# Performance work log

Measured on AMD Instinct MI355X. Metric: run time of the kernel, lower is better.

Reference implementation:

```python
import jax, jax.numpy as jnp
import numpy as np

VOCAB, EMB, HID, TEMP = 10000, 256, 512, 0.5
EPS = 1e-20


def _lstm(x_seq, h0, c0, Wih, Whh, b):
    # x_seq: [T, B, E]; PyTorch gate order i, f, g, o
    def step(carry, x):
        h, c = carry
        gates = x @ Wih + h @ Whh + b
        i, f, g, o = jnp.split(gates, 4, axis=-1)
        c = jax.nn.sigmoid(f) * c + jax.nn.sigmoid(i) * jnp.tanh(g)
        h = jax.nn.sigmoid(o) * jnp.tanh(c)
        return (h, c), h
    (hT, cT), hs = jax.lax.scan(step, (h0, c0), x_seq)
    return hs, hT, cT


def setup_inputs() -> dict:
    key = jax.random.key(0)
    ks = jax.random.split(key, 16)
    B, T = 32, 128
    s = 0.02
    input_ids = jax.random.randint(ks[0], (B, T), 0, VOCAB, dtype=jnp.int32)
    mask = jax.random.randint(ks[1], (B, T), 0, 2, dtype=jnp.int32)
    U = jax.random.uniform(ks[2], (T, B, VOCAB), dtype=jnp.float32)
    gumbel_noise = -jnp.log(-jnp.log(U + EPS) + EPS)
    return {
        'input_ids': input_ids,
        'my_attention_mask': mask,
        'enc_embed': s * jax.random.normal(ks[3], (VOCAB, EMB), jnp.float32),
        'enc_Wih': s * jax.random.normal(ks[4], (EMB, 4 * HID), jnp.float32),
        'enc_Whh': s * jax.random.normal(ks[5], (HID, 4 * HID), jnp.float32),
        'enc_b': jnp.zeros((4 * HID,), jnp.float32),
        'dec_embed': s * jax.random.normal(ks[6], (VOCAB, EMB), jnp.float32),
        'dec_Wih': s * jax.random.normal(ks[7], (EMB, 4 * HID), jnp.float32),
        'dec_Whh': s * jax.random.normal(ks[8], (HID, 4 * HID), jnp.float32),
        'dec_b': jnp.zeros((4 * HID,), jnp.float32),
        'fc_W': s * jax.random.normal(ks[9], (HID, VOCAB), jnp.float32),
        'fc_b': jnp.zeros((VOCAB,), jnp.float32),
        'rand_init': jax.random.uniform(ks[10], (T, B, VOCAB), dtype=jnp.float32),
        'gumbel_noise': gumbel_noise,
    }


def reference(input_ids, my_attention_mask, enc_embed, enc_Wih, enc_Whh, enc_b,
              dec_embed, dec_Wih, dec_Whh, dec_b, fc_W, fc_b,
              rand_init, gumbel_noise):
    B, T = input_ids.shape
    mask = my_attention_mask                      # [B, T]
    tokens = input_ids.T                          # [T, B] (torch.t of view)

    h0 = jnp.zeros((B, HID), jnp.float32)
    # Encoder over full sequence
    _, hT, cT = _lstm(enc_embed[tokens], h0, h0, enc_Wih, enc_Whh, enc_b)
    # Decoder: teacher-forced on tokens[0:T-1] -> outputs for steps t=1..T-1
    hs, _, _ = _lstm(dec_embed[tokens[:-1]], hT, cT, dec_Wih, dec_Whh, dec_b)
    logits = hs @ fc_W + fc_b                     # [T-1, B, V]

    # Mask-driven compaction: outputs[sum(mask[j,:t]), j] = logits[t-1, j] where mask[j,t]==1
    excl = jnp.cumsum(mask, axis=1) - mask        # exclusive prefix sum [B, T]
    pos = excl[:, 1:]                             # [B, T-1]
    valid = mask[:, 1:] > 0
    pos_use = jnp.where(valid, pos, T)            # out-of-range -> dropped
    jj = jnp.broadcast_to(jnp.arange(B)[:, None], pos_use.shape)
    outputs = rand_init.at[pos_use, jj].set(jnp.swapaxes(logits, 0, 1), mode='drop')  # [T, B, V]

    # Hard gumbel-softmax with straight-through
    y = jax.nn.softmax((outputs + gumbel_noise) / TEMP, axis=-1)
    y_hard = jax.nn.one_hot(jnp.argmax(y, axis=-1), VOCAB, dtype=y.dtype)
    gs = jax.lax.stop_gradient(y_hard - y) + y    # [T, B, V]

    # Re-expand: masked positions take compacted gumbel rows, unmasked take token one-hots
    gathered = gs[excl, jnp.arange(B)[:, None]]   # [B, T, V]
    tok_oh = jax.nn.one_hot(input_ids, VOCAB, dtype=jnp.float32)
    onehots = jnp.where((mask > 0)[..., None], gathered, tok_oh)  # [B, T, V]
    return onehots.reshape(-1, VOCAB)             # dense form of the sparse inputs_embeds
```

## Files before the change

kernel.cpp:

```cpp
#include <hip/hip_runtime.h>
#include <hip/hip_bf16.h>
#include <math.h>

#define BB 32
#define TT 128
#define TD 127
#define EMB 256
#define HID 512
#define G4 2048
#define NV 10000
#define NB 64
#define UPB 8

typedef __attribute__((ext_vector_type(8))) short short8v;
typedef __attribute__((ext_vector_type(4))) float f32x4;

__device__ __forceinline__ unsigned short bf16_rne(float x){
    unsigned int u = __float_as_uint(x);
    u += 0x7fffu + ((u >> 16) & 1u);
    return (unsigned short)(u >> 16);
}
__device__ __forceinline__ float bf16f(unsigned short h){
    return __uint_as_float(((unsigned int)h) << 16);
}

__global__ __launch_bounds__(256) void gemm_x(const int* __restrict__ ids,
        const float* __restrict__ embed, const float* __restrict__ W,
        const float* __restrict__ bias, float* __restrict__ X, int M)
{
    __shared__ float As[16][128];
    __shared__ float Bs[16][128];
    __shared__ int toks[128];
    const int tid = threadIdx.x;
    const int m0 = blockIdx.y * 128, n0 = blockIdx.x * 128;
    if (tid < 128) {
        int mr = m0 + tid, tk = 0;
        if (mr < M) { int t = mr >> 5, b = mr & 31; tk = ids[b*TT + t]; }
        toks[tid] = tk;
    }
    __syncthreads();
    float acc[8][8] = {};
    const int ty = tid >> 4, tx = tid & 15;
    for (int kt = 0; kt < EMB; kt += 16) {
        #pragma unroll
        for (int i = 0; i < 2; i++) {
            int idx = tid*2 + i;
            int row = idx >> 2, k4 = (idx & 3)*4;
            float4 a = *(const float4*)&embed[(size_t)toks[row]*EMB + kt + k4];
            As[k4+0][row] = a.x; As[k4+1][row] = a.y; As[k4+2][row] = a.z; As[k4+3][row] = a.w;
        }
        #pragma unroll
        for (int i = 0; i < 2; i++) {
            int idx = tid*2 + i;
            int kr = idx >> 5, c4 = (idx & 31)*4;
            *(float4*)&Bs[kr][c4] = *(const float4*)&W[(size_t)(kt+kr)*G4 + n0 + c4];
        }
        __syncthreads();
        #pragma unroll
        for (int k = 0; k < 16; k++) {
            float a8[8], b8[8];
            #pragma unroll
            for (int i = 0; i < 8; i++) a8[i] = As[k][ty*8+i];
            #pragma unroll
            for (int j = 0; j < 8; j++) b8[j] = Bs[k][tx*8+j];
            #pragma unroll
            for (int i = 0; i < 8; i++) {
                #pragma unroll
                for (int j = 0; j < 8; j++)
                    acc[i][j] = fmaf(a8[i], b8[j], acc[i][j]);
            }
        }
        __syncthreads();
    }
    #pragma unroll
    for (int i = 0; i < 8; i++) {
        int mr = m0 + ty*8 + i;
        if (mr < M) {
            int tt = mr >> 5, bb2 = mr & 31;
            #pragma unroll
            for (int j = 0; j < 8; j++) {
                int nc = n0 + tx*8 + j;
                X[((size_t)tt*G4 + nc)*BB + bb2] = acc[i][j] + bias[nc];
            }
        }
    }
}

__global__ __launch_bounds__(512) void lstm_persist(
        const float* __restrict__ Xenc, const float* __restrict__ Xdec,
        const float* __restrict__ Whh_e, const float* __restrict__ Whh_d,
        unsigned int* __restrict__ h_pk,
        float* __restrict__ hs,
        int* __restrict__ flags)
{
    __shared__ float smem[10272];
    float* partials = smem;
    float* xbuf     = smem + 9216;

    const int tid = threadIdx.x;
    const int bid = blockIdx.x;
    const int u0  = bid*UPB;
    const int w   = tid >> 6;
    const int l   = tid & 63;
    const int rl  = l & 15;
    const int kg  = (l >> 4) * 8;
    const int r4  = (l >> 4) * 4;

    short8v wH_n0k0, wH_n0k1, wH_n1k0, wH_n1k1;
    short8v wL_n0k0, wL_n0k1, wL_n1k0, wL_n1k1;

    #define BW(WH, WL, KB, CO) do { _Pragma("unroll") \
        for (int j = 0; j < 8; ++j) { \
            float wv = partials[((KB)+j)*32 + (CO) + rl]; \
            unsigned short h2 = bf16_rne(wv); \
            WH[j] = (short)h2; \
            WL[j] = (short)bf16_rne(wv - bf16f(h2)); \
        } } while(0)

    #define STAGE_BUILD(SRC) do { \
        for (int c = 0; c < 4; ++c) { \
            int k0 = c*128; \
            __syncthreads(); \
            for (int i = tid; i < 4096; i += 512) { \
                int kl = i >> 5, n = i & 31; \
                partials[kl*32 + n] = SRC[(size_t)(k0+kl)*G4 + (size_t)((n>>3)*512 + u0 + (n&7))]; \
            } \
            __syncthreads(); \
            if ((w >> 1) == c) { \
                int kb0 = w*64 - k0 + kg; \
                BW(wH_n0k0, wL_n0k0, kb0,      0); \
                BW(wH_n0k1, wL_n0k1, kb0 + 32, 0); \
                BW(wH_n1k0, wL_n1k0, kb0,     16); \
                BW(wH_n1k1, wL_n1k1, kb0 + 32,16); \
            } \
        } \
        __syncthreads(); } while(0)

    STAGE_BUILD(Whh_e);

    {
        for (int i = tid; i < 1024; i += 512) {
            int row = i & 31, n = i >> 5;
            xbuf[row*33 + n] = Xenc[(size_t)((n>>3)*512 + u0 + (n&7))*32 + row];
        }
        __syncthreads();
    }

    float c_reg = 0.f;
    const int gb = tid >> 3, gul = tid & 7;

    for (int gstep = 0; gstep < TT + TD; ++gstep) {
        const bool enc = gstep < TT;
        const int t = enc ? gstep : gstep - TT;

        f32x4 acc00 = {0,0,0,0}, acc01 = {0,0,0,0}, acc10 = {0,0,0,0}, acc11 = {0,0,0,0};
        if (gstep > 0) {
            const unsigned int* hp = h_pk + (size_t)(gstep & 1)*16384;
            short8v aH_m0k0, aH_m0k1, aH_m1k0, aH_m1k1;
            short8v aL_m0k0, aL_m0k1, aL_m1k0, aL_m1k1;
            #define LOAD_A(AH, AL, MT, KS) do { \
                unsigned int pv[8]; \
                int kbase = w*64 + (KS)*32 + kg; \
                int brow = (MT)*16 + rl; \
                _Pragma("unroll") \
                for (int j = 0; j < 8; ++j) \
                    pv[j] = __hip_atomic_load(&hp[(kbase+j)*32 + brow], \
                                __ATOMIC_RELAXED, __HIP_MEMORY_SCOPE_AGENT); \
                _Pragma("unroll") \
                for (int j = 0; j < 8; ++j) { \
                    AH[j] = (short)(pv[j] & 0xffffu); \
                    AL[j] = (short)(pv[j] >> 16); \
                } } while(0)
            LOAD_A(aH_m0k0, aL_m0k0, 0, 0); LOAD_A(aH_m0k1, aL_m0k1, 0, 1);
            LOAD_A(aH_m1k0, aL_m1k0, 1, 0); LOAD_A(aH_m1k1, aL_m1k1, 1, 1);
            #define MM6(ACC, AH0, AH1, AL0, AL1, WH0, WH1, WL0, WL1) do { \
                ACC = __builtin_amdgcn_mfma_f32_16x16x32_bf16(AH0, WH0, ACC, 0,0,0); \
                ACC = __builtin_amdgcn_mfma_f32_16x16x32_bf16(AH1, WH1, ACC, 0,0,0); \
                ACC = __builtin_amdgcn_mfma_f32_16x16x32_bf16(AL0, WH0, ACC, 0,0,0); \
                ACC = __builtin_amdgcn_mfma_f32_16x16x32_bf16(AL1, WH1, ACC, 0,0,0); \
                ACC = __builtin_amdgcn_mfma_f32_16x16x32_bf16(AH0, WL0, ACC, 0,0,0); \
                ACC = __builtin_amdgcn_mfma_f32_16x16x32_bf16(AH1, WL1, ACC, 0,0,0); \
            } while(0)
            MM6(acc00, aH_m0k0, aH_m0k1, aL_m0k0, aL_m0k1, wH_n0k0, wH_n0k1, wL_n0k0, wL_n0k1);
            MM6(acc01, aH_m0k0, aH_m0k1, aL_m0k0, aL_m0k1, wH_n1k0, wH_n1k1, wL_n1k0, wL_n1k1);
            MM6(acc10, aH_m1k0, aH_m1k1, aL_m1k0, aL_m1k1, wH_n0k0, wH_n0k1, wL_n0k0, wL_n0k1);
            MM6(acc11, aH_m1k0, aH_m1k1, aL_m1k0, aL_m1k1, wH_n1k0, wH_n1k1, wL_n1k0, wL_n1k1);
        }
        #pragma unroll
        for (int j = 0; j < 4; ++j) {
            partials[(w*32 +      r4 + j)*36 +      rl] = acc00[j];
            partials[(w*32 +      r4 + j)*36 + 16 + rl] = acc01[j];
            partials[(w*32 + 16 + r4 + j)*36 +      rl] = acc10[j];
            partials[(w*32 + 16 + r4 + j)*36 + 16 + rl] = acc11[j];
        }
        __syncthreads();

        float hv = 0.f;
        if (tid < 256) {
            float pre[4];
            #pragma unroll
            for (int g = 0; g < 4; ++g) {
                float s = xbuf[gb*33 + g*8 + gul];
                #pragma unroll
                for (int ww = 0; ww < 8; ++ww)
                    s += partials[(ww*32 + gb)*36 + g*8 + gul];
                pre[g] = s;
            }
            float iv = 1.f/(1.f + expf(-pre[0]));
            float fv = 1.f/(1.f + expf(-pre[1]));
            float gv = tanhf(pre[2]);
            float ov = 1.f/(1.f + expf(-pre[3]));
            c_reg = fmaf(fv, c_reg, iv*gv);
            hv = ov * tanhf(c_reg);
            unsigned short hh = bf16_rne(hv);
            unsigned short hl = bf16_rne(hv - bf16f(hh));
            unsigned int pk = (unsigned int)hh | ((unsigned int)hl << 16);
            __hip_atomic_store(&h_pk[(size_t)((gstep+1) & 1)*16384 + (u0+gul)*32 + gb],
                               pk, __ATOMIC_RELAXED, __HIP_MEMORY_SCOPE_AGENT);
        }
        __syncthreads();
        if (gstep < TT + TD - 1 && tid == 0)
            __hip_atomic_store(&flags[bid], gstep + 1,
                               __ATOMIC_RELAXED, __HIP_MEMORY_SCOPE_AGENT);
        if (!enc && tid < 256)
            hs[((size_t)t*BB + gb)*HID + u0 + gul] = hv;
        if (gstep == TT + TD - 1) break;

        if (gstep == TT - 1) STAGE_BUILD(Whh_d);

        {
            int tn = gstep + 1 < TT ? gstep + 1 : gstep + 1 - TT;
            const float* Xt = (gstep + 1 < TT ? Xenc : Xdec) + (size_t)tn*G4*BB;
            for (int i = tid; i < 1024; i += 512) {
                int row = i & 31, n = i >> 5;
                xbuf[row*33 + n] = Xt[(size_t)((n>>3)*512 + u0 + (n&7))*32 + row];
            }
        }
        if (tid < NB) {
            while (__hip_atomic_load(&flags[tid], __ATOMIC_RELAXED,
                                     __HIP_MEMORY_SCOPE_AGENT) <= gstep) {}
        }
        __syncthreads();
        asm volatile("" ::: "memory");
    }
}

__global__ void transpose_fc(const float* __restrict__ W, float* __restrict__ Wt)
{
    __shared__ float tile[32][33];
    int v0 = blockIdx.x*32, k0 = blockIdx.y*32;
    int tx = threadIdx.x, ty = threadIdx.y;
    #pragma unroll
    for (int r = 0; r < 32; r += 8) {
        int k = k0 + ty + r, v = v0 + tx;
        tile[ty+r][tx] = (v < NV) ? W[(size_t)k*NV + v] : 0.f;
    }
    __syncthreads();
    #pragma unroll
    for (int r = 0; r < 32; r += 8) {
        int v = v0 + ty + r, k = k0 + tx;
        if (v < NV) Wt[(size_t)v*HID + k] = tile[tx][ty+r];
    }
}

__global__ void wnorm(const float* __restrict__ W, const float* __restrict__ bvec,
                      unsigned int* __restrict__ scal)
{
    int v = blockIdx.x*256 + threadIdx.x;
    if (v < NV) {
        float s = 0.f;
        for (int k = 0; k < HID; k++) { float w = W[(size_t)k*NV + v]; s = fmaf(w, w, s); }
        atomicMax(&scal[0], __float_as_uint(s));
        atomicMax(&scal[1], __float_as_uint(fabsf(bvec[v])));
    }
}

__global__ void hnorm(const float* __restrict__ hs, unsigned int* __restrict__ scal)
{
    int r = blockIdx.x, lane = threadIdx.x;
    float s = 0.f;
    for (int k = lane; k < HID; k += 64) { float x = hs[(size_t)r*HID + k]; s = fmaf(x, x, s); }
    for (int o = 32; o; o >>= 1) s += __shfl_down(s, o);
    if (lane == 0) atomicMax(&scal[2], __float_as_uint(s));
}

__global__ void routing(const int* __restrict__ ids, const int* __restrict__ mask,
                        int* __restrict__ exclk, int* __restrict__ winner)
{
    int b = blockIdx.x;
    __shared__ int pre[TT];
    int t = threadIdx.x;
    if (t == 0) { int s = 0; for (int i = 0; i < TT; i++) { pre[i] = s; s += mask[b*TT+i]; } }
    __syncthreads();
    exclk[b*TT + t] = pre[t];
    if (mask[b*TT + t] == 0) winner[b*TT + t] = ids[b*TT + t];
}

__global__ __launch_bounds__(256) void rowmax(const int* __restrict__ mask,
        const int* __restrict__ exclk, const float* __restrict__ gum, float* __restrict__ Mr)
{
    int row = blockIdx.x, b = row >> 7, t = row & 127;
    if (t == 0 || mask[row] == 0) return;
    int k = exclk[row];
    const float* g = gum + ((size_t)k*BB + b)*NV;
    float m = -1e30f;
    for (int v = threadIdx.x; v < NV; v += 256) m = fmaxf(m, g[v]);
    __shared__ float red[256];
    red[threadIdx.x] = m; __syncthreads();
    for (int s = 128; s; s >>= 1) {
        if (threadIdx.x < s) red[threadIdx.x] = fmaxf(red[threadIdx.x], red[threadIdx.x+s]);
        __syncthreads();
    }
    if (threadIdx.x == 0) Mr[row] = red[0];
}

__global__ __launch_bounds__(256) void cand_argmax(const int* __restrict__ mask,
        const int* __restrict__ exclk, const float* __restrict__ gum,
        const float* __restrict__ rinit, const float* __restrict__ hs,
        const float* __restrict__ Wt, const float* __restrict__ fcb,
        const float* __restrict__ Mr, const unsigned int* __restrict__ scal,
        int* __restrict__ winner)
{
    int row = blockIdx.x, b = row >> 7, t = row & 127;
    if (mask[row] == 0) return;
    int tid = threadIdx.x;
    __shared__ float red[256];
    __shared__ int idxr[256];
    __shared__ int list[256];
    __shared__ int wcnt[4];

    if (t == 0) {
        const float* g  = gum   + (size_t)b*NV;
        const float* r0 = rinit + (size_t)b*NV;
        float bs = -1e30f; int bv = 0x7fffffff;
        for (int v = tid; v < NV; v += 256) {
            float sc = r0[v] + g[v];
            if (sc > bs) { bs = sc; bv = v; }
        }
        red[tid] = bs; idxr[tid] = bv; __syncthreads();
        for (int s = 128; s; s >>= 1) {
            if (tid < s) {
                if (red[tid+s] > red[tid] || (red[tid+s] == red[tid] && idxr[tid+s] < idxr[tid])) {
                    red[tid] = red[tid+s]; idxr[tid] = idxr[tid+s];
                }
            }
            __syncthreads();
        }
        if (tid == 0) winner[row] = idxr[0];
        return;
    }

    int k = exclk[row];
    const float* g    = gum + ((size_t)k*BB + b)*NV;
    const float* hrow = hs + ((size_t)(t-1)*BB + b)*HID;
    float bound = sqrtf(__uint_as_float(scal[0])) * sqrtf(__uint_as_float(scal[2]))
                + __uint_as_float(scal[1]);
    float thr = Mr[row] - 2.0f*bound*1.05f - 1e-6f;

    float curS = -1e30f; int curV = 0x7fffffff;
    int wv = tid >> 6, lane = tid & 63;
    for (int v0 = 0; v0 < NV; v0 += 256) {
        int v = v0 + tid;
        bool ok = (v < NV) && (g[v] >= thr);
        unsigned long long mb = __ballot(ok);
        if (lane == 0) wcnt[wv] = __popcll(mb);
        __syncthreads();
        int off = 0;
        #pragma unroll
        for (int w = 0; w < 4; w++) if (w < wv) off += wcnt[w];
        int tot = wcnt[0] + wcnt[1] + wcnt[2] + wcnt[3];
        if (ok) {
            int pos = off + __popcll(mb & ((1ull << lane) - 1ull));
            list[pos] = v;
        }
        __syncthreads();
        for (int ci = 0; ci < tot; ci++) {
            int vc = list[ci];
            float p = 0.f;
            for (int k2 = tid; k2 < HID; k2 += 256)
                p = fmaf(hrow[k2], Wt[(size_t)vc*HID + k2], p);
            red[tid] = p; __syncthreads();
            for (int s = 128; s; s >>= 1) {
                if (tid < s) red[tid] += red[tid+s];
                __syncthreads();
            }
            if (tid == 0) {
                float sc = (red[0] + fcb[vc]) + g[vc];
                if (sc > curS || (sc == curS && vc < curV)) { curS = sc; curV = vc; }
            }
            __syncthreads();
        }
    }
    if (tid == 0) winner[row] = curV;
}

__global__ __launch_bounds__(256) void write_out(const int* __restrict__ winner,
                                                 float* __restrict__ out)
{
    int row = blockIdx.x;
    int win = winner[row];
    float4* o = (float4*)(out + (size_t)row*NV);
    int tid = threadIdx.x;
    #pragma unroll
    for (int i = 0; i < 10; i++) {
        int idx = tid + i*256;
        if (idx < 2500) {
            int vb = idx*4;
            float4 val = {0.f, 0.f, 0.f, 0.f};
            if (win >= vb && win < vb+4) ((float*)&val)[win - vb] = 1.0f;
            o[idx] = val;
        }
    }
}

extern "C" void kernel_launch(void* const* d_in, const int* in_sizes, int n_in,
                              void* d_out, int out_size, void* d_ws, size_t ws_size,
                              hipStream_t stream)
{
    const int*   ids   = (const int*)d_in[0];
    const int*   mask  = (const int*)d_in[1];
    const float* eEmb  = (const float*)d_in[2];
    const float* eWih  = (const float*)d_in[3];
    const float* eWhh  = (const float*)d_in[4];
    const float* eB    = (const float*)d_in[5];
    const float* dEmb  = (const float*)d_in[6];
    const float* dWih  = (const float*)d_in[7];
    const float* dWhh  = (const float*)d_in[8];
    const float* dB    = (const float*)d_in[9];
    const float* fcW   = (const float*)d_in[10];
    const float* fcb   = (const float*)d_in[11];
    const float* rinit = (const float*)d_in[12];
    const float* gum   = (const float*)d_in[13];
    float* out = (float*)d_out;

    float* wsf = (float*)d_ws;
    size_t off = 0;
    float* Xenc = wsf + off; off += (size_t)TT*BB*G4;
    float* Xdec = wsf + off; off += (size_t)TD*BB*G4;
    unsigned int* h_pk = (unsigned int*)(wsf + off); off += 2*(size_t)BB*HID;
    float* hs   = wsf + off; off += (size_t)TD*BB*HID;
    float* fcWt = wsf + off; off += (size_t)NV*HID;
    float* Mr   = wsf + off; off += 4096;
    unsigned int* scal = (unsigned int*)(wsf + off); off += 8;
    int* flags  = (int*)(wsf + off); off += NB;
    int* exclk  = (int*)(wsf + off); off += 4096;
    int* winner = (int*)(wsf + off); off += 4096;

    hipMemsetAsync(scal,  0, 8*sizeof(int), stream);
    hipMemsetAsync(flags, 0, NB*sizeof(int), stream);

    dim3 gblk(16, 32);
    gemm_x<<<gblk, 256, 0, stream>>>(ids, eEmb, eWih, eB, Xenc, TT*BB);
    gemm_x<<<gblk, 256, 0, stream>>>(ids, dEmb, dWih, dB, Xdec, TD*BB);
    transpose_fc<<<dim3(313,16), dim3(32,8), 0, stream>>>(fcW, fcWt);
    wnorm<<<40, 256, 0, stream>>>(fcW, fcb, scal);
    routing<<<32, 128, 0, stream>>>(ids, mask, exclk, winner);

    lstm_persist<<<NB, 512, 0, stream>>>(Xenc, Xdec, eWhh, dWhh, h_pk, hs, flags);

    hnorm<<<TD*BB, 64, 0, stream>>>(hs, scal);
    rowmax<<<4096, 256, 0, stream>>>(mask, exclk, gum, Mr);
    cand_argmax<<<4096, 256, 0, stream>>>(mask, exclk, gum, rinit, hs, fcWt, fcb, Mr, scal, winner);
    write_out<<<4096, 256, 0, stream>>>(winner, out);
}
```

Before: 1.152 ms.

## Overlap independent precompute with persistent LSTM via worker blocks in same launch

Adds 192 worker blocks to the persistent LSTM grid. While the recurrent blocks run the encoder, the workers do the decoder input GEMM, the fc weight transpose, the weight norm and the gumbel row maxima. The LSTM blocks wait on a completion counter before they read decoder inputs, and the x-buffer is now double-buffered. Routing, hnorm, candidate argmax and output write are merged into one kernel that computes a per-row h norm bound. This removes several launches and their serial tails, at the risk that the workers contend with the latency-sensitive recurrent blocks or that the grid does not fit co-resident.

New measurement: 1.004 ms. -12.8%, faster.

```diff
diff --git a/kernel.cpp b/kernel.cpp
--- a/kernel.cpp
+++ b/kernel.cpp
@@ -10,7 +10,16 @@
 #define G4 2048
 #define NV 10000
 #define NB 64
+#define NWK 192
+#define GRID_UBER (NB + NWK)
 #define UPB 8
+#define NT_STEPS (TT + TD)
+
+#define NJOB_DEC 512
+#define NJOB_TR  313
+#define NJOB_WN  20
+#define NJOB_RM  4096
+#define NJOBS (NJOB_DEC + NJOB_TR + NJOB_WN + NJOB_RM)
 
 typedef __attribute__((ext_vector_type(8))) short short8v;
 typedef __attribute__((ext_vector_type(4))) float f32x4;
@@ -87,34 +96,162 @@
 }
 
 __global__ __launch_bounds__(512) void lstm_persist(
-        const float* __restrict__ Xenc, const float* __restrict__ Xdec,
+        const float* __restrict__ Xenc, float* __restrict__ Xdec,
         const float* __restrict__ Whh_e, const float* __restrict__ Whh_d,
         unsigned int* __restrict__ h_pk,
         float* __restrict__ hs,
-        int* __restrict__ flags)
+        int* __restrict__ flags,
+        int* __restrict__ decdone,
+        const int* __restrict__ ids, const float* __restrict__ dEmb,
+        const float* __restrict__ dWih, const float* __restrict__ dB,
+        const float* __restrict__ fcW, float* __restrict__ fcWt,
+        const float* __restrict__ fcb, const int* __restrict__ mask,
+        const float* __restrict__ gum, float* __restrict__ Mr,
+        unsigned int* __restrict__ scal)
 {
-    __shared__ float smem[10272];
+    __shared__ float smem[11392];
+    const int tid = threadIdx.x;
+    const int bid = blockIdx.x;
+
+    if (bid >= NB) {
+        const int wid = bid - NB;
+        for (int job = wid; job < NJOBS; job += NWK) {
+            if (job < NJOB_DEC) {
+                const int my = job >> 4, nx = job & 15;
+                const int m0 = my*128, n0 = nx*128;
+                const int M = TD*BB;
+                float* As = smem;
+                float* Bs = smem + 2048;
+                int* toks = (int*)(smem + 4096);
+                if (tid < 128) {
+                    int mr = m0 + tid, tk = 0;
+                    if (mr < M) { int t = mr >> 5, b2 = mr & 31; tk = ids[b2*TT + t]; }
+                    toks[tid] = tk;
+                }
+                __syncthreads();
+                float acc[4][8] = {};
+                const int ty = tid >> 4, tx = tid & 15;
+                for (int kt = 0; kt < EMB; kt += 16) {
+                    {
+                        int row = tid >> 2, k4 = (tid & 3)*4;
+                        float4 a = *(const float4*)&dEmb[(size_t)toks[row]*EMB + kt + k4];
+                        As[(k4+0)*128+row] = a.x; As[(k4+1)*128+row] = a.y;
+                        As[(k4+2)*128+row] = a.z; As[(k4+3)*128+row] = a.w;
+                    }
+                    {
+                        int kr = tid >> 5, c4 = (tid & 31)*4;
+                        *(float4*)&Bs[kr*128 + c4] =
+                            *(const float4*)&dWih[(size_t)(kt+kr)*G4 + n0 + c4];
+                    }
+                    __syncthreads();
+                    #pragma unroll
+                    for (int k = 0; k < 16; k++) {
+                        float a4[4], b8[8];
+                        #pragma unroll
+                        for (int i = 0; i < 4; i++) a4[i] = As[k*128 + ty*4+i];
+                        #pragma unroll
+                        for (int j = 0; j < 8; j++) b8[j] = Bs[k*128 + tx*8+j];
+                        #pragma unroll
+                        for (int i = 0; i < 4; i++) {
+                            #pragma unroll
+                            for (int j = 0; j < 8; j++)
+                                acc[i][j] = fmaf(a4[i], b8[j], acc[i][j]);
+                        }
+                    }
+                    __syncthreads();
+                }
+                #pragma unroll
+                for (int i = 0; i < 4; i++) {
+                    int mr = m0 + ty*4 + i;
+                    if (mr < M) {
+                        int t = mr >> 5, b2 = mr & 31;
+                        #pragma unroll
+                        for (int j = 0; j < 8; j++) {
+                            int nc = n0 + tx*8 + j;
+                            Xdec[((size_t)t*G4 + nc)*BB + b2] = acc[i][j] + dB[nc];
+                        }
+                    }
+                }
+                __syncthreads();
+                if (tid == 0)
+                    __hip_atomic_fetch_add(decdone, 1,
+                        __ATOMIC_RELEASE, __HIP_MEMORY_SCOPE_AGENT);
+            } else if (job < NJOB_DEC + NJOB_TR) {
+                const int v0 = (job - NJOB_DEC)*32;
+                float* tile = smem;
+                for (int k0 = 0; k0 < HID; k0 += 16) {
+                    {
+                        int kk = tid >> 5, vv = tid & 31;
+                        int v = v0 + vv;
+                        tile[kk*33 + vv] = (v < NV) ? fcW[(size_t)(k0+kk)*NV + v] : 0.f;
+                    }
+                    __syncthreads();
+                    {
+                        int vy = tid >> 4, kx = tid & 15;
+                        int v = v0 + vy;
+                        if (v < NV) fcWt[(size_t)v*HID + k0 + kx] = tile[kx*33 + vy];
+                    }
+                    __syncthreads();
+                }
+            } else if (job < NJOB_DEC + NJOB_TR + NJOB_WN) {
+                int v = (job - NJOB_DEC - NJOB_TR)*512 + tid;
+                if (v < NV) {
+                    float s = 0.f;
+                    for (int k = 0; k < HID; k++) {
+                        float x = fcW[(size_t)k*NV + v]; s = fmaf(x, x, s);
+                    }
+                    atomicMax(&scal[0], __float_as_uint(s));
+                    atomicMax(&scal[1], __float_as_uint(fabsf(fcb[v])));
+                }
+            } else {
+                const int row = job - NJOB_DEC - NJOB_TR - NJOB_WN;
+                const int b = row >> 7, t = row & 127;
+                const int mrow = mask[row];
+                if (t != 0 && mrow != 0) {
+                    int* wk = (int*)&smem[520];
+                    int mi = (tid < TT) ? mask[b*TT + tid] : 0;
+                    unsigned long long bal = __ballot(tid < t && mi != 0);
+                    if ((tid & 63) == 0) wk[tid >> 6] = __popcll(bal);
+                    __syncthreads();
+                    int k = wk[0] + wk[1];
+                    __syncthreads();
+                    const float* g = gum + ((size_t)k*BB + b)*NV;
+                    float m = -1e30f;
+                    for (int v = tid; v < NV; v += 512) m = fmaxf(m, g[v]);
+                    float* red = smem;
+                    red[tid] = m; __syncthreads();
+                    for (int s = 256; s; s >>= 1) {
+                        if (tid < s) red[tid] = fmaxf(red[tid], red[tid+s]);
+                        __syncthreads();
+                    }
+                    if (tid == 0) Mr[row] = red[0];
+                    __syncthreads();
+                }
+            }
+        }
+        return;
+    }
+
     float* partials = smem;
     float* xbuf     = smem + 9216;
 
-    const int tid = threadIdx.x;
-    const int bid = blockIdx.x;
     const int u0  = bid*UPB;
     const int w   = tid >> 6;
     const int l   = tid & 63;
     const int rl  = l & 15;
     const int kg  = (l >> 4) * 8;
     const int r4  = (l >> 4) * 4;
+    const int gb  = tid >> 3, gul = tid & 7;
 
     short8v wH_n0k0, wH_n0k1, wH_n1k0, wH_n1k1;
     short8v wL_n0k0, wL_n0k1, wL_n1k0, wL_n1k1;
 
     #define BW(WH, WL, KB, CO) do { _Pragma("unroll") \
         for (int j = 0; j < 8; ++j) { \
-            float wv = partials[((KB)+j)*32 + (CO) + rl]; \
-            unsigned short h2 = bf16_rne(wv); \
-            WH[j] = (short)h2; \
-            WL[j] = (short)bf16_rne(wv - bf16f(h2)); \
+            float wv2 = partials[((KB)+j)*32 + (CO) + rl]; \
+            unsigned short htop = bf16_rne(wv2); \
+            WH[j] = (short)htop; \
+            WL[j] = (short)bf16_rne(wv2 - bf16f(htop)); \
         } } while(0)
 
     #define STAGE_BUILD(SRC) do { \
@@ -140,16 +277,24 @@
 
     {
         for (int i = tid; i < 1024; i += 512) {
-            int row = i & 31, n = i >> 5;
-            xbuf[row*33 + n] = Xenc[(size_t)((n>>3)*512 + u0 + (n&7))*32 + row];
+            int row2 = i & 31, n = i >> 5;
+            xbuf[row2*33 + n] = Xenc[(size_t)((n>>3)*512 + u0 + (n&7))*32 + row2];
         }
         __syncthreads();
     }
 
     float c_reg = 0.f;
-    const int gb = tid >> 3, gul = tid & 7;
-
-    for (int gstep = 0; gstep < TT + TD; ++gstep) {
+
+    #define MM6(ACC, AH0, AH1, AL0, AL1, WH0, WH1, WL0, WL1) do { \
+        ACC = __builtin_amdgcn_mfma_f32_16x16x32_bf16(AH0, WH0, ACC, 0,0,0); \
+        ACC = __builtin_amdgcn_mfma_f32_16x16x32_bf16(AH1, WH1, ACC, 0,0,0); \
+        ACC = __builtin_amdgcn_mfma_f32_16x16x32_bf16(AL0, WH0, ACC, 0,0,0); \
+        ACC = __builtin_amdgcn_mfma_f32_16x16x32_bf16(AL1, WH1, ACC, 0,0,0); \
+        ACC = __builtin_amdgcn_mfma_f32_16x16x32_bf16(AH0, WL0, ACC, 0,0,0); \
+        ACC = __builtin_amdgcn_mfma_f32_16x16x32_bf16(AH1, WL1, ACC, 0,0,0); \
+    } while(0)
+
+    for (int gstep = 0; gstep < NT_STEPS; ++gstep) {
         const bool enc = gstep < TT;
         const int t = enc ? gstep : gstep - TT;
 
@@ -173,14 +318,6 @@
                 } } while(0)
             LOAD_A(aH_m0k0, aL_m0k0, 0, 0); LOAD_A(aH_m0k1, aL_m0k1, 0, 1);
             LOAD_A(aH_m1k0, aL_m1k0, 1, 0); LOAD_A(aH_m1k1, aL_m1k1, 1, 1);
-            #define MM6(ACC, AH0, AH1, AL0, AL1, WH0, WH1, WL0, WL1) do { \
-                ACC = __builtin_amdgcn_mfma_f32_16x16x32_bf16(AH0, WH0, ACC, 0,0,0); \
-                ACC = __builtin_amdgcn_mfma_f32_16x16x32_bf16(AH1, WH1, ACC, 0,0,0); \
-                ACC = __builtin_amdgcn_mfma_f32_16x16x32_bf16(AL0, WH0, ACC, 0,0,0); \
-                ACC = __builtin_amdgcn_mfma_f32_16x16x32_bf16(AL1, WH1, ACC, 0,0,0); \
-                ACC = __builtin_amdgcn_mfma_f32_16x16x32_bf16(AH0, WL0, ACC, 0,0,0); \
-                ACC = __builtin_amdgcn_mfma_f32_16x16x32_bf16(AH1, WL1, ACC, 0,0,0); \
-            } while(0)
             MM6(acc00, aH_m0k0, aH_m0k1, aL_m0k0, aL_m0k1, wH_n0k0, wH_n0k1, wL_n0k0, wL_n0k1);
             MM6(acc01, aH_m0k0, aH_m0k1, aL_m0k0, aL_m0k1, wH_n1k0, wH_n1k1, wL_n1k0, wL_n1k1);
             MM6(acc10, aH_m1k0, aH_m1k1, aL_m1k0, aL_m1k1, wH_n0k0, wH_n0k1, wL_n0k0, wL_n0k1);
@@ -199,12 +336,12 @@
         if (tid < 256) {
             float pre[4];
             #pragma unroll
-            for (int g = 0; g < 4; ++g) {
-                float s = xbuf[gb*33 + g*8 + gul];
+            for (int gg = 0; gg < 4; ++gg) {
+                float s = xbuf[(gstep & 1)*1056 + gb*33 + gg*8 + gul];
                 #pragma unroll
                 for (int ww = 0; ww < 8; ++ww)
-                    s += partials[(ww*32 + gb)*36 + g*8 + gul];
-                pre[g] = s;
+                    s += partials[(ww*32 + gb)*36 + gg*8 + gul];
+                pre[gg] = s;
             }
             float iv = 1.f/(1.f + expf(-pre[0]));
             float fv = 1.f/(1.f + expf(-pre[1]));
@@ -219,21 +356,31 @@
                                pk, __ATOMIC_RELAXED, __HIP_MEMORY_SCOPE_AGENT);
         }
         __syncthreads();
-        if (gstep < TT + TD - 1 && tid == 0)
+        if (gstep < NT_STEPS - 1 && tid == 0)
             __hip_atomic_store(&flags[bid], gstep + 1,
                                __ATOMIC_RELAXED, __HIP_MEMORY_SCOPE_AGENT);
         if (!enc && tid < 256)
             hs[((size_t)t*BB + gb)*HID + u0 + gul] = hv;
-        if (gstep == TT + TD - 1) break;
+        if (gstep == NT_STEPS - 1) break;
 
         if (gstep == TT - 1) STAGE_BUILD(Whh_d);
 
         {
+            if (gstep + 1 == TT) {
+                if (tid == 0) {
+                    while (__hip_atomic_load(decdone, __ATOMIC_RELAXED,
+                                             __HIP_MEMORY_SCOPE_AGENT) < NJOB_DEC)
+                        __builtin_amdgcn_s_sleep(8);
+                }
+                __syncthreads();
+                __builtin_amdgcn_fence(__ATOMIC_ACQUIRE, "agent");
+            }
             int tn = gstep + 1 < TT ? gstep + 1 : gstep + 1 - TT;
-            const float* Xt = (gstep + 1 < TT ? Xenc : Xdec) + (size_t)tn*G4*BB;
+            const float* Xt = (gstep + 1 < TT ? Xenc : (const float*)Xdec) + (size_t)tn*G4*BB;
             for (int i = tid; i < 1024; i += 512) {
-                int row = i & 31, n = i >> 5;
-                xbuf[row*33 + n] = Xt[(size_t)((n>>3)*512 + u0 + (n&7))*32 + row];
+                int row2 = i & 31, n = i >> 5;
+                xbuf[((gstep+1) & 1)*1056 + row2*33 + n] =
+                    Xt[(size_t)((n>>3)*512 + u0 + (n&7))*32 + row2];
             }
         }
         if (tid < NB) {
@@ -245,91 +392,25 @@
     }
 }
 
-__global__ void transpose_fc(const float* __restrict__ W, float* __restrict__ Wt)
+__global__ __launch_bounds__(256) void cand_write(
+        const int* __restrict__ ids, const int* __restrict__ mask,
+        const float* __restrict__ gum, const float* __restrict__ rinit,
+        const float* __restrict__ hs, const float* __restrict__ Wt,
+        const float* __restrict__ fcb, const float* __restrict__ Mr,
+        const unsigned int* __restrict__ scal, float* __restrict__ out)
 {
-    __shared__ float tile[32][33];
-    int v0 = blockIdx.x*32, k0 = blockIdx.y*32;
-    int tx = threadIdx.x, ty = threadIdx.y;
-    #pragma unroll
-    for (int r = 0; r < 32; r += 8) {
-        int k = k0 + ty + r, v = v0 + tx;
-        tile[ty+r][tx] = (v < NV) ? W[(size_t)k*NV + v] : 0.f;
-    }
-    __syncthreads();
-    #pragma unroll
-    for (int r = 0; r < 32; r += 8) {
-        int v = v0 + ty + r, k = k0 + tx;
-        if (v < NV) Wt[(size_t)v*HID + k] = tile[tx][ty+r];
-    }
-}
-
-__global__ void wnorm(const float* __restrict__ W, const float* __restrict__ bvec,
-                      unsigned int* __restrict__ scal)
-{
-    int v = blockIdx.x*256 + threadIdx.x;
-    if (v < NV) {
-        float s = 0.f;
-        for (int k = 0; k < HID; k++) { float w = W[(size_t)k*NV + v]; s = fmaf(w, w, s); }
-        atomicMax(&scal[0], __float_as_uint(s));
-        atomicMax(&scal[1], __float_as_uint(fabsf(bvec[v])));
-    }
-}
-
-__global__ void hnorm(const float* __restrict__ hs, unsigned int* __restrict__ scal)
-{
-    int r = blockIdx.x, lane = threadIdx.x;
-    float s = 0.f;
-    for (int k = lane; k < HID; k += 64) { float x = hs[(size_t)r*HID + k]; s = fmaf(x, x, s); }
-    for (int o = 32; o; o >>= 1) s += __shfl_down(s, o);
-    if (lane == 0) atomicMax(&scal[2], __float_as_uint(s));
-}
-
-__global__ void routing(const int* __restrict__ ids, const int* __restrict__ mask,
-                        int* __restrict__ exclk, int* __restrict__ winner)
-{
-    int b = blockIdx.x;
-    __shared__ int pre[TT];
-    int t = threadIdx.x;
-    if (t == 0) { int s = 0; for (int i = 0; i < TT; i++) { pre[i] = s; s += mask[b*TT+i]; } }
-    __syncthreads();
-    exclk[b*TT + t] = pre[t];
-    if (mask[b*TT + t] == 0) winner[b*TT + t] = ids[b*TT + t];
-}
-
-__global__ __launch_bounds__(256) void rowmax(const int* __restrict__ mask,
-        const int* __restrict__ exclk, const float* __restrict__ gum, float* __restrict__ Mr)
-{
-    int row = blockIdx.x, b = row >> 7, t = row & 127;
-    if (t == 0 || mask[row] == 0) return;
-    int k = exclk[row];
-    const float* g = gum + ((size_t)k*BB + b)*NV;
-    float m = -1e30f;
-    for (int v = threadIdx.x; v < NV; v += 256) m = fmaxf(m, g[v]);
-    __shared__ float red[256];
-    red[threadIdx.x] = m; __syncthreads();
-    for (int s = 128; s; s >>= 1) {
-        if (threadIdx.x < s) red[threadIdx.x] = fmaxf(red[threadIdx.x], red[threadIdx.x+s]);
-        __syncthreads();
-    }
-    if (threadIdx.x == 0) Mr[row] = red[0];
-}
-
-__global__ __launch_bounds__(256) void cand_argmax(const int* __restrict__ mask,
-        const int* __restrict__ exclk, const float* __restrict__ gum,
-        const float* __restrict__ rinit, const float* __restrict__ hs,
-        const float* __restrict__ Wt, const float* __restrict__ fcb,
-        const float* __restrict__ Mr, const unsigned int* __restrict__ scal,
-        int* __restrict__ winner)
-{
-    int row = blockIdx.x, b = row >> 7, t = row & 127;
-    if (mask[row] == 0) return;
-    int tid = threadIdx.x;
+    const int row = blockIdx.x, b = row >> 7, t = row & 127;
+    const int tid = threadIdx.x;
     __shared__ float red[256];
     __shared__ int idxr[256];
     __shared__ int list[256];
     __shared__ int wcnt[4];
-
-    if (t == 0) {
+    __shared__ int winsh;
+
+    int win;
+    if (mask[row] == 0) {
+        win = ids[b*TT + t];
+    } else if (t == 0) {
         const float* g  = gum   + (size_t)b*NV;
         const float* r0 = rinit + (size_t)b*NV;
         float bs = -1e30f; int bv = 0x7fffffff;
@@ -346,61 +427,69 @@
             }
             __syncthreads();
         }
-        if (tid == 0) winner[row] = idxr[0];
-        return;
-    }
-
-    int k = exclk[row];
-    const float* g    = gum + ((size_t)k*BB + b)*NV;
-    const float* hrow = hs + ((size_t)(t-1)*BB + b)*HID;
-    float bound = sqrtf(__uint_as_float(scal[0])) * sqrtf(__uint_as_float(scal[2]))
-                + __uint_as_float(scal[1]);
-    float thr = Mr[row] - 2.0f*bound*1.05f - 1e-6f;
-
-    float curS = -1e30f; int curV = 0x7fffffff;
-    int wv = tid >> 6, lane = tid & 63;
-    for (int v0 = 0; v0 < NV; v0 += 256) {
-        int v = v0 + tid;
-        bool ok = (v < NV) && (g[v] >= thr);
-        unsigned long long mb = __ballot(ok);
-        if (lane == 0) wcnt[wv] = __popcll(mb);
-        __syncthreads();
-        int off = 0;
-        #pragma unroll
-        for (int w = 0; w < 4; w++) if (w < wv) off += wcnt[w];
-        int tot = wcnt[0] + wcnt[1] + wcnt[2] + wcnt[3];
-        if (ok) {
-            int pos = off + __popcll(mb & ((1ull << lane) - 1ull));
-            list[pos] = v;
-        }
-        __syncthreads();
-        for (int ci = 0; ci < tot; ci++) {
-            int vc = list[ci];
-            float p = 0.f;
-            for (int k2 = tid; k2 < HID; k2 += 256)
-                p = fmaf(hrow[k2], Wt[(size_t)vc*HID + k2], p);
-            red[tid] = p; __syncthreads();
-            for (int s = 128; s; s >>= 1) {
-                if (tid < s) red[tid] += red[tid+s];
+        win = idxr[0];
+    } else {
+        int mi = (tid < TT) ? mask[b*TT + tid] : 0;
+        unsigned long long bal = __ballot(tid < t && mi != 0);
+        if ((tid & 63) == 0) wcnt[tid >> 6] = __popcll(bal);
+        __syncthreads();
+        const int k = wcnt[0] + wcnt[1];
+        __syncthreads();
+
+        const float* g    = gum + ((size_t)k*BB + b)*NV;
+        const float* hrow = hs + ((size_t)(t-1)*BB + b)*HID;
+        float hn = 0.f;
+        for (int k2 = tid; k2 < HID; k2 += 256) { float x = hrow[k2]; hn = fmaf(x, x, hn); }
+        red[tid] = hn; __syncthreads();
+        for (int s = 128; s; s >>= 1) {
+            if (tid < s) red[tid] += red[tid+s];
+            __syncthreads();
+        }
+        float bound = sqrtf(__uint_as_float(scal[0])) * sqrtf(red[0])
+                    + __uint_as_float(scal[1]);
+        float thr = Mr[row] - 2.0f*bound*1.05f - 1e-6f;
+        __syncthreads();
+
+        float curS = -1e30f; int curV = 0x7fffffff;
+        int wv = tid >> 6, lane = tid & 63;
+        for (int v0 = 0; v0 < NV; v0 += 256) {
+            int v = v0 + tid;
+            bool ok = (v < NV) && (g[v] >= thr);
+            unsigned long long mb = __ballot(ok);
+            if (lane == 0) wcnt[wv] = __popcll(mb);
+            __syncthreads();
+            int off = 0;
+            #pragma unroll
+            for (int w = 0; w < 4; w++) if (w < wv) off += wcnt[w];
+            int tot = wcnt[0] + wcnt[1] + wcnt[2] + wcnt[3];
+            if (ok) {
+                int pos = off + __popcll(mb & ((1ull << lane) - 1ull));
+                list[pos] = v;
+            }
+            __syncthreads();
+            for (int ci = 0; ci < tot; ci++) {
+                int vc = list[ci];
+                float p = 0.f;
+                for (int k2 = tid; k2 < HID; k2 += 256)
+                    p = fmaf(hrow[k2], Wt[(size_t)vc*HID + k2], p);
+                red[tid] = p; __syncthreads();
+                for (int s = 128; s; s >>= 1) {
+                    if (tid < s) red[tid] += red[tid+s];
+                    __syncthreads();
+                }
+                if (tid == 0) {
+                    float sc = (red[0] + fcb[vc]) + g[vc];
+                    if (sc > curS || (sc == curS && vc < curV)) { curS = sc; curV = vc; }
+                }
                 __syncthreads();
             }
-            if (tid == 0) {
-                float sc = (red[0] + fcb[vc]) + g[vc];
-                if (sc > curS || (sc == curS && vc < curV)) { curS = sc; curV = vc; }
-            }
-            __syncthreads();
-        }
-    }
-    if (tid == 0) winner[row] = curV;
-}
-
-__global__ __launch_bounds__(256) void write_out(const int* __restrict__ winner,
-                                                 float* __restrict__ out)
-{
-    int row = blockIdx.x;
-    int win = winner[row];
+        }
+        if (tid == 0) winsh = curV;
+        __syncthreads();
+        win = winsh;
+    }
+
     float4* o = (float4*)(out + (size_t)row*NV);
-    int tid = threadIdx.x;
     #pragma unroll
     for (int i = 0; i < 10; i++) {
         int idx = tid + i*256;
@@ -441,25 +530,20 @@
     float* hs   = wsf + off; off += (size_t)TD*BB*HID;
     float* fcWt = wsf + off; off += (size_t)NV*HID;
     float* Mr   = wsf + off; off += 4096;
-    unsigned int* scal = (unsigned int*)(wsf + off); off += 8;
-    int* flags  = (int*)(wsf + off); off += NB;
-    int* exclk  = (int*)(wsf + off); off += 4096;
-    int* winner = (int*)(wsf + off); off += 4096;
-
-    hipMemsetAsync(scal,  0, 8*sizeof(int), stream);
-    hipMemsetAsync(flags, 0, NB*sizeof(int), stream);
+    unsigned int* ctl = (unsigned int*)(wsf + off); off += 128;
+    unsigned int* scal = ctl;
+    int* flags   = (int*)(ctl + 8);
+    int* decdone = (int*)(ctl + 72);
+
+    hipMemsetAsync(ctl, 0, 128*sizeof(int), stream);
 
     dim3 gblk(16, 32);
     gemm_x<<<gblk, 256, 0, stream>>>(ids, eEmb, eWih, eB, Xenc, TT*BB);
-    gemm_x<<<gblk, 256, 0, stream>>>(ids, dEmb, dWih, dB, Xdec, TD*BB);
-    transpose_fc<<<dim3(313,16), dim3(32,8), 0, stream>>>(fcW, fcWt);
-    wnorm<<<40, 256, 0, stream>>>(fcW, fcb, scal);
-    routing<<<32, 128, 0, stream>>>(ids, mask, exclk, winner);
-
-    lstm_persist<<<NB, 512, 0, stream>>>(Xenc, Xdec, eWhh, dWhh, h_pk, hs, flags);
-
-    hnorm<<<TD*BB, 64, 0, stream>>>(hs, scal);
-    rowmax<<<4096, 256, 0, stream>>>(mask, exclk, gum, Mr);
-    cand_argmax<<<4096, 256, 0, stream>>>(mask, exclk, gum, rinit, hs, fcWt, fcb, Mr, scal, winner);
-    write_out<<<4096, 256, 0, stream>>>(winner, out);
+
+    lstm_persist<<<GRID_UBER, 512, 0, stream>>>(Xenc, Xdec, eWhh, dWhh,
+        h_pk, hs, flags, decdone,
+        ids, dEmb, dWih, dB, fcW, fcWt, fcb, mask, gum, Mr, scal);
+
+    cand_write<<<4096, 256, 0, stream>>>(ids, mask, gum, rinit, hs, fcWt, fcb,
+                                         Mr, scal, out);
 }
```
